# Performance work log

Hardware: AMD Instinct MI355X
Metric: run time of the kernel (lower is better)

## Reference

```python
import jax, jax.numpy as jnp
import numpy as np

N_R = 256          # number of relations
N_HOP_MAX = 3      # max hops
N_E = 200_000      # number of entities
N_T = 1_000_000    # number of KB triples
B = 32             # batch size
D_Q = 768          # BERT question embedding dim
D_IN = D_Q + (N_HOP_MAX - 1) * N_R  # input width of dense_inf / dense_att


def setup_inputs() -> dict:
    key = jax.random.key(0)
    ks = jax.random.split(key, 7)
    x = (jax.random.uniform(ks[0], (B, N_E)) < 0.001).astype(jnp.float32)
    h_q = jax.random.normal(ks[1], (B, D_Q), jnp.float32)
    W_inf = jax.random.normal(ks[2], (N_R, D_IN), jnp.float32) * 0.02
    W_att = jax.random.normal(ks[3], (1, D_IN), jnp.float32) * 0.02
    subj_idx = jax.random.randint(ks[4], (N_T,), 0, N_E, jnp.int32)
    rel_idx = jax.random.randint(ks[5], (N_T,), 0, N_R, jnp.int32)
    obj_idx = jax.random.randint(ks[6], (N_T,), 0, N_E, jnp.int32)
    return {"x": x, "h_q": h_q, "W_inf": W_inf, "W_att": W_att,
            "subj_idx": subj_idx, "rel_idx": rel_idx, "obj_idx": obj_idx,
            "n_hop": N_HOP_MAX}


def _one_step(x, r, subj_idx, rel_idx, obj_idx):
    # Equivalent to ((x @ M_subj.T) * (r @ M_rel.T)) @ M_obj with 0/1
    # indicator matrices: gather - elementwise multiply - scatter-add.
    x_t = jnp.take(x, subj_idx, axis=1)   # (B, N_T)
    r_t = jnp.take(r, rel_idx, axis=1)    # (B, N_T)
    prod = x_t * r_t                       # (B, N_T)
    # scatter-add over triples into object entities: (N_T, B) -> (N_E, B)
    return jax.ops.segment_sum(prod.T, obj_idx, num_segments=x.shape[1]).T


def reference(x, h_q, W_inf, W_att, subj_idx, rel_idx, obj_idx, n_hop):
    rs, cs, xs = [], [], []
    for i in range(n_hop):
        if i:
            # most-recent relation first, then older ones (rs[::-1])
            concat = jnp.concatenate([h_q] + rs[::-1], axis=1)
        else:
            concat = h_q
        pad = jnp.zeros((h_q.shape[0], (N_HOP_MAX - 1 - i) * N_R), h_q.dtype)
        concat = jnp.concatenate([concat, pad], axis=1)  # (B, D_IN)
        r = concat @ W_inf.T   # (B, N_R)
        c = concat @ W_att.T   # (B, 1)
        x = _one_step(x, r, subj_idx, rel_idx, obj_idx)  # (B, N_E)
        rs.append(r)
        cs.append(c)
        xs.append(x)
    a = jax.nn.softmax(jnp.concatenate(cs, axis=1), axis=-1)  # (B, n_hop)
    y = jnp.einsum('bh,bhe->be', a, jnp.stack(xs, axis=1))     # (B, N_E)
    return y
```

## Files before the change

kernel.cpp:

```cpp
#include <hip/hip_runtime.h>

#define N_R   256
#define N_E   200000
#define N_T   1000000
#define D_Q   768
#define D_IN  1280
#define NHB   3907
#define NBW   6256

template <bool BN>
__device__ __forceinline__ void hop_one(
        const float* __restrict__ xIn, const unsigned* __restrict__ maskIn,
        const unsigned* __restrict__ bitIn, const float* __restrict__ rT,
        const int* __restrict__ subj, const int* __restrict__ rel,
        const int* __restrict__ obj,
        float* __restrict__ xOut, unsigned* __restrict__ maskOut,
        unsigned* __restrict__ bitOut, int tid) {
    if (tid >= N_T) return;
    int s = subj[tid];
    unsigned gw = bitIn[s >> 5];
    if (!((gw >> (s & 31)) & 1)) return;
    int r = rel[tid];
    int o = obj[tid];
    unsigned mm = maskIn[s];
    atomicOr(&maskOut[o], mm);
    atomicOr(&bitOut[o >> 5], 1u << (o & 31));
    const float* rrow = rT + r * 32;
    while (mm) {
        int bb = __ffs(mm) - 1;
        mm &= mm - 1;
        float v = BN ? xIn[(size_t)bb * N_E + s] : xIn[(size_t)s * 32 + bb];
        unsafeAtomicAdd(&xOut[(size_t)o * 32 + bb], v * rrow[bb]);
    }
}

__global__ void kA(const float* __restrict__ x, const float* __restrict__ h_q,
                   const float* __restrict__ W_inf,
                   unsigned* __restrict__ mask0, unsigned* __restrict__ mask1,
                   unsigned* __restrict__ mask2,
                   unsigned* __restrict__ bit0, unsigned* __restrict__ bit1,
                   unsigned* __restrict__ bit2,
                   float4* __restrict__ outv, float* __restrict__ rT0) {
    __shared__ float hs[32 * 257];
    __shared__ float red[256];
    int t = threadIdx.x;
    if (blockIdx.x < 782) {
        int tid = blockIdx.x * 256 + t;
        float4 z = {0.f, 0.f, 0.f, 0.f};
        for (int i = tid; i < 1600000; i += 782 * 256) outv[i] = z;
        if (tid < NBW) { bit1[tid] = 0u; bit2[tid] = 0u; }
        unsigned m = 0;
        if (tid < N_E) {
#pragma unroll 8
            for (int b = 0; b < 32; ++b)
                m |= (x[(size_t)b * N_E + tid] != 0.f ? 1u : 0u) << b;
        }
        unsigned long long bal = __ballot(m != 0u);
        int lane = t & 63;
        if (lane == 0)  bit0[tid >> 5] = (unsigned)bal;
        if (lane == 32) bit0[tid >> 5] = (unsigned)(bal >> 32);
        if (tid < N_E) {
            mask0[tid] = m;
            mask1[tid] = 0u;
            mask2[tid] = 0u;
        }
    } else {
        int rel = blockIdx.x - 782;
        int b = t & 31, kp = t >> 5;
        float acc = 0.f;
        for (int c = 0; c < 3; ++c) {
            __syncthreads();
#pragma unroll
            for (int i = 0; i < 32; ++i)
                hs[i * 257 + t] = h_q[i * D_Q + c * 256 + t];
            __syncthreads();
            const float* w = &W_inf[rel * D_IN + c * 256 + kp * 32];
#pragma unroll
            for (int i = 0; i < 32; ++i)
                acc += w[i] * hs[b * 257 + kp * 32 + i];
        }
        red[t] = acc;
        __syncthreads();
        if (t < 32) {
            float s = 0.f;
            for (int q = 0; q < 8; ++q) s += red[q * 32 + t];
            rT0[rel * 32 + t] = s;
        }
    }
}

__global__ void kB(const float* __restrict__ W_inf, const float* __restrict__ rT0,
                   float* __restrict__ rT1,
                   const float* __restrict__ x, const unsigned* __restrict__ mask0,
                   const unsigned* __restrict__ bit0,
                   const int* __restrict__ subj, const int* __restrict__ rel,
                   const int* __restrict__ obj,
                   float* __restrict__ bufA, unsigned* __restrict__ mask1,
                   unsigned* __restrict__ bit1) {
    __shared__ float red[256];
    int t = threadIdx.x;
    if (blockIdx.x < 256) {
        int relb = blockIdx.x;
        int b = t & 31, jp = t >> 5;
        const float* w2 = &W_inf[relb * D_IN + D_Q];
        float acc = 0.f;
#pragma unroll 8
        for (int jj = 0; jj < 32; ++jj) {
            int j = jp * 32 + jj;
            acc += w2[j] * rT0[j * 32 + b];
        }
        red[t] = acc;
        __syncthreads();
        if (t < 32) {
            float s = rT0[relb * 32 + t];
            for (int q = 0; q < 8; ++q) s += red[q * 32 + t];
            rT1[relb * 32 + t] = s;
        }
    } else {
        hop_one<true>(x, mask0, bit0, rT0, subj, rel, obj, bufA, mask1, bit1,
                      (blockIdx.x - 256) * 256 + t);
    }
}

__global__ void kC(const float* __restrict__ W_inf, const float* __restrict__ W_att,
                   const float* __restrict__ h_q,
                   const float* __restrict__ rT0, const float* __restrict__ rT1,
                   float* __restrict__ rT2, float* __restrict__ a_w,
                   const float* __restrict__ bufA, const unsigned* __restrict__ mask1,
                   const unsigned* __restrict__ bit1,
                   const int* __restrict__ subj, const int* __restrict__ rel,
                   const int* __restrict__ obj,
                   float* __restrict__ bufB, unsigned* __restrict__ mask2,
                   unsigned* __restrict__ bit2) {
    __shared__ float red[256];
    __shared__ float p0[256], p1[256], p2[256], p3[256];
    int t = threadIdx.x;
    if (blockIdx.x < 256) {
        int relb = blockIdx.x;
        int b = t & 31, jp = t >> 5;
        const float* w2 = &W_inf[relb * D_IN + D_Q];
        const float* w3 = w2 + N_R;
        float acc = 0.f;
#pragma unroll 8
        for (int jj = 0; jj < 32; ++jj) {
            int j = jp * 32 + jj;
            acc += w2[j] * rT1[j * 32 + b] + w3[j] * rT0[j * 32 + b];
        }
        red[t] = acc;
        __syncthreads();
        if (t < 32) {
            float s = rT0[relb * 32 + t];
            for (int q = 0; q < 8; ++q) s += red[q * 32 + t];
            rT2[relb * 32 + t] = s;
        }
    } else if (blockIdx.x == 256) {
        int b = t & 31, p = t >> 5;
        float c0 = 0.f;
        for (int k = p * 96; k < p * 96 + 96; ++k) c0 += W_att[k] * h_q[b * D_Q + k];
        float s1 = 0.f, s2 = 0.f, s3 = 0.f;
        for (int j = p * 32; j < p * 32 + 32; ++j) {
            float w2 = W_att[D_Q + j], w3 = W_att[D_Q + N_R + j];
            float r0v = rT0[j * 32 + b], r1v = rT1[j * 32 + b];
            s1 += w2 * r0v; s2 += w2 * r1v; s3 += w3 * r0v;
        }
        p0[t] = c0; p1[t] = s1; p2[t] = s2; p3[t] = s3;
        __syncthreads();
        if (t < 32) {
            float C0 = 0.f, S1 = 0.f, S2 = 0.f, S3 = 0.f;
            for (int q = 0; q < 8; ++q) {
                C0 += p0[q * 32 + t]; S1 += p1[q * 32 + t];
                S2 += p2[q * 32 + t]; S3 += p3[q * 32 + t];
            }
            float c1 = C0 + S1, c2 = C0 + S2 + S3;
            float m  = fmaxf(C0, fmaxf(c1, c2));
            float e0 = __expf(C0 - m), e1 = __expf(c1 - m), e2 = __expf(c2 - m);
            float inv = 1.f / (e0 + e1 + e2);
            a_w[t] = e0 * inv; a_w[32 + t] = e1 * inv; a_w[64 + t] = e2 * inv;
        }
    } else {
        hop_one<false>(bufA, mask1, bit1, rT1, subj, rel, obj, bufB, mask2, bit2,
                       (blockIdx.x - 257) * 256 + t);
    }
}

__global__ void kDE(const float* __restrict__ bufA, const float* __restrict__ bufB,
                    const unsigned* __restrict__ mask1,
                    const unsigned* __restrict__ mask2,
                    const unsigned* __restrict__ bit2,
                    const float* __restrict__ rT2, const float* __restrict__ a_w,
                    const int* __restrict__ subj, const int* __restrict__ rel,
                    const int* __restrict__ obj, float* __restrict__ out) {
    __shared__ float a0s[32], a1s[32], a2s[32];
    int t = threadIdx.x;
    if (t < 32) { a0s[t] = a_w[t]; a1s[t] = a_w[32 + t]; a2s[t] = a_w[64 + t]; }
    __syncthreads();
    if (blockIdx.x < NHB) {
        int tid = blockIdx.x * 256 + t;
        if (tid >= N_T) return;
        int s = subj[tid];
        int r = rel[tid];
        int o = obj[tid];
        unsigned gw = bit2[s >> 5];
        if (!((gw >> (s & 31)) & 1)) return;
        unsigned mm = mask2[s];
        const float* rrow = rT2 + r * 32;
        const float* xrow = bufB + (size_t)s * 32;
        while (mm) {
            int bb = __ffs(mm) - 1;
            mm &= mm - 1;
            unsafeAtomicAdd(&out[(size_t)bb * N_E + o],
                            a2s[bb] * xrow[bb] * rrow[bb]);
        }
    } else {
        int e = (blockIdx.x - NHB) * 256 + t;
        if (e >= N_E) return;
        unsigned m1v = mask1[e], m2v = mask2[e];
        unsigned mu = m1v | m2v;
        if (!mu) return;
        const float* r1 = bufA + (size_t)e * 32;
        const float* r2 = bufB + (size_t)e * 32;
        while (mu) {
            int bb = __ffs(mu) - 1;
            mu &= mu - 1;
            float c = 0.f;
            if ((m1v >> bb) & 1) c += a0s[bb] * r1[bb];
            if ((m2v >> bb) & 1) c += a1s[bb] * r2[bb];
            unsafeAtomicAdd(&out[(size_t)bb * N_E + e], c);
        }
    }
}

extern "C" void kernel_launch(void* const* d_in, const int* in_sizes, int n_in,
                              void* d_out, int out_size, void* d_ws, size_t ws_size,
                              hipStream_t stream) {
    const float* x     = (const float*)d_in[0];
    const float* h_q   = (const float*)d_in[1];
    const float* W_inf = (const float*)d_in[2];
    const float* W_att = (const float*)d_in[3];
    const int*   subj  = (const int*)d_in[4];
    const int*   rel   = (const int*)d_in[5];
    const int*   obj   = (const int*)d_in[6];
    float* out = (float*)d_out;

    const size_t NEB = (size_t)N_E * 32;
    float*    bufA  = (float*)d_ws;
    float*    bufB  = bufA + NEB;
    float*    rT0   = bufB + NEB;
    float*    rT1   = rT0 + N_R * 32;
    float*    rT2   = rT1 + N_R * 32;
    float*    a_w   = rT2 + N_R * 32;
    unsigned* mask0 = (unsigned*)(a_w + 96);
    unsigned* mask1 = mask0 + N_E;
    unsigned* mask2 = mask1 + N_E;
    unsigned* bit0  = mask2 + N_E;
    unsigned* bit1  = bit0 + NBW;
    unsigned* bit2  = bit1 + NBW;

    kA<<<782 + 256, 256, 0, stream>>>(x, h_q, W_inf, mask0, mask1, mask2,
                                      bit0, bit1, bit2, (float4*)out, rT0);
    kB<<<256 + NHB, 256, 0, stream>>>(W_inf, rT0, rT1, x, mask0, bit0,
                                      subj, rel, obj, bufA, mask1, bit1);
    kC<<<257 + NHB, 256, 0, stream>>>(W_inf, W_att, h_q, rT0, rT1, rT2, a_w,
                                      bufA, mask1, bit1, subj, rel, obj,
                                      bufB, mask2, bit2);
    kDE<<<NHB + 782, 256, 0, stream>>>(bufA, bufB, mask1, mask2, bit2, rT2, a_w,
                                       subj, rel, obj, out);
}
```

Before: 194.3 us.

## Drop bitset prefilter and move output zeroing into the hop-2 kernel

Removes the per-entity active bitsets (bit0/1/2) and their atomicOr maintenance, and instead filters triples by loading the 32-bit batch mask for the subject directly. The 6.4 MB output zero-fill moves from kA into the hop-2 blocks of kC, spreading it over more blocks that are mostly idle after their early exit. This saves a ballot, the bitset writes and atomics, but every triple now does a scattered 4-byte mask load instead of a compact bitset read that stays cache-resident.

```diff
diff --git a/kernel.cpp b/kernel.cpp
--- a/kernel.cpp
+++ b/kernel.cpp
@@ -6,25 +6,21 @@
 #define D_Q   768
 #define D_IN  1280
 #define NHB   3907
-#define NBW   6256
 
 template <bool BN>
 __device__ __forceinline__ void hop_one(
         const float* __restrict__ xIn, const unsigned* __restrict__ maskIn,
-        const unsigned* __restrict__ bitIn, const float* __restrict__ rT,
+        const float* __restrict__ rT,
         const int* __restrict__ subj, const int* __restrict__ rel,
         const int* __restrict__ obj,
-        float* __restrict__ xOut, unsigned* __restrict__ maskOut,
-        unsigned* __restrict__ bitOut, int tid) {
+        float* __restrict__ xOut, unsigned* __restrict__ maskOut, int tid) {
     if (tid >= N_T) return;
     int s = subj[tid];
-    unsigned gw = bitIn[s >> 5];
-    if (!((gw >> (s & 31)) & 1)) return;
     int r = rel[tid];
     int o = obj[tid];
     unsigned mm = maskIn[s];
+    if (!mm) return;
     atomicOr(&maskOut[o], mm);
-    atomicOr(&bitOut[o >> 5], 1u << (o & 31));
     const float* rrow = rT + r * 32;
     while (mm) {
         int bb = __ffs(mm) - 1;
@@ -37,29 +33,17 @@
 __global__ void kA(const float* __restrict__ x, const float* __restrict__ h_q,
                    const float* __restrict__ W_inf,
                    unsigned* __restrict__ mask0, unsigned* __restrict__ mask1,
-                   unsigned* __restrict__ mask2,
-                   unsigned* __restrict__ bit0, unsigned* __restrict__ bit1,
-                   unsigned* __restrict__ bit2,
-                   float4* __restrict__ outv, float* __restrict__ rT0) {
+                   unsigned* __restrict__ mask2, float* __restrict__ rT0) {
     __shared__ float hs[32 * 257];
     __shared__ float red[256];
     int t = threadIdx.x;
     if (blockIdx.x < 782) {
         int tid = blockIdx.x * 256 + t;
-        float4 z = {0.f, 0.f, 0.f, 0.f};
-        for (int i = tid; i < 1600000; i += 782 * 256) outv[i] = z;
-        if (tid < NBW) { bit1[tid] = 0u; bit2[tid] = 0u; }
-        unsigned m = 0;
         if (tid < N_E) {
+            unsigned m = 0;
 #pragma unroll 8
             for (int b = 0; b < 32; ++b)
                 m |= (x[(size_t)b * N_E + tid] != 0.f ? 1u : 0u) << b;
-        }
-        unsigned long long bal = __ballot(m != 0u);
-        int lane = t & 63;
-        if (lane == 0)  bit0[tid >> 5] = (unsigned)bal;
-        if (lane == 32) bit0[tid >> 5] = (unsigned)(bal >> 32);
-        if (tid < N_E) {
             mask0[tid] = m;
             mask1[tid] = 0u;
             mask2[tid] = 0u;
@@ -92,11 +76,9 @@
 __global__ void kB(const float* __restrict__ W_inf, const float* __restrict__ rT0,
                    float* __restrict__ rT1,
                    const float* __restrict__ x, const unsigned* __restrict__ mask0,
-                   const unsigned* __restrict__ bit0,
                    const int* __restrict__ subj, const int* __restrict__ rel,
                    const int* __restrict__ obj,
-                   float* __restrict__ bufA, unsigned* __restrict__ mask1,
-                   unsigned* __restrict__ bit1) {
+                   float* __restrict__ bufA, unsigned* __restrict__ mask1) {
     __shared__ float red[256];
     int t = threadIdx.x;
     if (blockIdx.x < 256) {
@@ -117,7 +99,7 @@
             rT1[relb * 32 + t] = s;
         }
     } else {
-        hop_one<true>(x, mask0, bit0, rT0, subj, rel, obj, bufA, mask1, bit1,
+        hop_one<true>(x, mask0, rT0, subj, rel, obj, bufA, mask1,
                       (blockIdx.x - 256) * 256 + t);
     }
 }
@@ -127,11 +109,10 @@
                    const float* __restrict__ rT0, const float* __restrict__ rT1,
                    float* __restrict__ rT2, float* __restrict__ a_w,
                    const float* __restrict__ bufA, const unsigned* __restrict__ mask1,
-                   const unsigned* __restrict__ bit1,
                    const int* __restrict__ subj, const int* __restrict__ rel,
                    const int* __restrict__ obj,
                    float* __restrict__ bufB, unsigned* __restrict__ mask2,
-                   unsigned* __restrict__ bit2) {
+                   float4* __restrict__ outv) {
     __shared__ float red[256];
     __shared__ float p0[256], p1[256], p2[256], p3[256];
     int t = threadIdx.x;
@@ -178,15 +159,17 @@
             a_w[t] = e0 * inv; a_w[32 + t] = e1 * inv; a_w[64 + t] = e2 * inv;
         }
     } else {
-        hop_one<false>(bufA, mask1, bit1, rT1, subj, rel, obj, bufB, mask2, bit2,
-                       (blockIdx.x - 257) * 256 + t);
+        int hb  = blockIdx.x - 257;
+        int tid = hb * 256 + t;
+        float4 z = {0.f, 0.f, 0.f, 0.f};
+        for (int i = tid; i < 1600000; i += NHB * 256) outv[i] = z;
+        hop_one<false>(bufA, mask1, rT1, subj, rel, obj, bufB, mask2, tid);
     }
 }
 
 __global__ void kDE(const float* __restrict__ bufA, const float* __restrict__ bufB,
                     const unsigned* __restrict__ mask1,
                     const unsigned* __restrict__ mask2,
-                    const unsigned* __restrict__ bit2,
                     const float* __restrict__ rT2, const float* __restrict__ a_w,
                     const int* __restrict__ subj, const int* __restrict__ rel,
                     const int* __restrict__ obj, float* __restrict__ out) {
@@ -200,9 +183,8 @@
         int s = subj[tid];
         int r = rel[tid];
         int o = obj[tid];
-        unsigned gw = bit2[s >> 5];
-        if (!((gw >> (s & 31)) & 1)) return;
         unsigned mm = mask2[s];
+        if (!mm) return;
         const float* rrow = rT2 + r * 32;
         const float* xrow = bufB + (size_t)s * 32;
         while (mm) {
@@ -252,17 +234,13 @@
     unsigned* mask0 = (unsigned*)(a_w + 96);
     unsigned* mask1 = mask0 + N_E;
     unsigned* mask2 = mask1 + N_E;
-    unsigned* bit0  = mask2 + N_E;
-    unsigned* bit1  = bit0 + NBW;
-    unsigned* bit2  = bit1 + NBW;
-
-    kA<<<782 + 256, 256, 0, stream>>>(x, h_q, W_inf, mask0, mask1, mask2,
-                                      bit0, bit1, bit2, (float4*)out, rT0);
-    kB<<<256 + NHB, 256, 0, stream>>>(W_inf, rT0, rT1, x, mask0, bit0,
-                                      subj, rel, obj, bufA, mask1, bit1);
+
+    kA<<<782 + 256, 256, 0, stream>>>(x, h_q, W_inf, mask0, mask1, mask2, rT0);
+    kB<<<256 + NHB, 256, 0, stream>>>(W_inf, rT0, rT1, x, mask0,
+                                      subj, rel, obj, bufA, mask1);
     kC<<<257 + NHB, 256, 0, stream>>>(W_inf, W_att, h_q, rT0, rT1, rT2, a_w,
-                                      bufA, mask1, bit1, subj, rel, obj,
-                                      bufB, mask2, bit2);
-    kDE<<<NHB + 782, 256, 0, stream>>>(bufA, bufB, mask1, mask2, bit2, rT2, a_w,
+                                      bufA, mask1, subj, rel, obj,
+                                      bufB, mask2, (float4*)out);
+    kDE<<<NHB + 782, 256, 0, stream>>>(bufA, bufB, mask1, mask2, rT2, a_w,
                                        subj, rel, obj, out);
 }
```

Result: faster. 187.1 us (-3.7%).
